# Kernel tuning notes

Measured on AMD Instinct MI355X. Metric: run time of the kernel, lower is better.

Reference implementation:

```python
import jax, jax.numpy as jnp
import numpy as np

EMBED = 200
ATT_D = 200
EPS = 1e-5


def _make_pos(x, embed_len):
    # p[i, j+off, k] = sin(j/1000^(j/E)) if k odd else cos(...); rows with leading
    # zero-count `off` get positions shifted right; first `off` rows stay zero.
    B, L = x.shape
    off = jnp.sum(x == 0, axis=1)                       # [B]
    j = jnp.arange(L)[None, :] - off[:, None]           # [B, L]
    valid = j >= 0
    jf = jnp.maximum(j, 0).astype(jnp.float32)
    angle = jf / jnp.power(1000.0, jf / embed_len)      # [B, L]
    kk = jnp.arange(embed_len)
    odd = (kk % 2 == 1)[None, None, :]
    val = jnp.where(odd, jnp.sin(angle)[:, :, None], jnp.cos(angle)[:, :, None])
    return jnp.where(valid[:, :, None], val, 0.0)       # [B, L, E]


def _ln2(y):
    # F.layer_norm over last TWO dims (seq, embed), no affine
    mu = jnp.mean(y, axis=(1, 2), keepdims=True)
    var = jnp.mean((y - mu) ** 2, axis=(1, 2), keepdims=True)
    return (y - mu) / jnp.sqrt(var + EPS)


def setup_inputs() -> dict:
    key = jax.random.key(0)
    ks = jax.random.split(key, 10)
    B, L, V = 32, 1024, 32000
    x = jax.random.randint(ks[0], (B, L), 0, V)
    embed = jax.random.normal(ks[1], (V, EMBED), dtype=jnp.float32) * 0.02
    w_qkv = jax.random.normal(ks[2], (EMBED, ATT_D), dtype=jnp.float32) * 0.02
    b_qkv = jnp.zeros((ATT_D,), dtype=jnp.float32)
    head = 8
    w_fuse = jax.random.normal(ks[3], (ATT_D * head, ATT_D), dtype=jnp.float32) * 0.02
    b_fuse = jnp.zeros((ATT_D,), dtype=jnp.float32)
    w1 = jax.random.normal(ks[4], (ATT_D, ATT_D), dtype=jnp.float32) * 0.02
    b1 = jnp.zeros((ATT_D,), dtype=jnp.float32)
    w2 = jax.random.normal(ks[5], (ATT_D, ATT_D), dtype=jnp.float32) * 0.02
    b2 = jnp.zeros((ATT_D,), dtype=jnp.float32)
    return {"x": x, "embed": embed, "w_qkv": w_qkv, "b_qkv": b_qkv,
            "w_fuse": w_fuse, "b_fuse": b_fuse, "w1": w1, "b1": b1,
            "w2": w2, "b2": b2, "stack": 6, "head": head}


def reference(x, embed, w_qkv, b_qkv, w_fuse, b_fuse, w1, b1, w2, b2, stack, head):
    p = _make_pos(x, EMBED)
    h = embed[x] + p                                     # [B, L, 200]
    scale = jnp.sqrt(jnp.float32(ATT_D))
    for _ in range(stack):
        r = h
        # q == k == v: the source shares ONE Linear across q/k/v, heads, stacks
        q = h @ w_qkv + b_qkv                            # [B, L, 200]
        d = jnp.einsum('bld,bmd->blm', q, q) / scale     # [B, L, L]
        a = jax.nn.softmax(d, axis=-1)
        c = jnp.einsum('blm,bmd->bld', a, q)             # [B, L, 200]
        c_all = jnp.tile(c, (1, 1, head))                # identical heads concat
        h = c_all @ w_fuse + b_fuse
        h = _ln2(h + r)
        r = h
        h = jax.nn.relu(h @ w1 + b1) @ w2 + b2
        h = _ln2(h + r)
    return h
```

## Files before the change

### kernel.cpp

```cpp
#include <hip/hip_runtime.h>
#include <hip/hip_bf16.h>

#define B_    32
#define L_    1024
#define D_    200
#define DP    256
#define M_    (B_*L_)
#define NTOT  (M_*DP)
#define NELEM 204800.f
#define INVSCALE 0.07071067811865475f
#define LNEPS 1e-5f

typedef unsigned short u16;
typedef unsigned int   u32;
typedef long long      i64;
typedef __attribute__((ext_vector_type(8))) short bf16x8;
typedef __attribute__((ext_vector_type(4))) float f32x4;

__device__ __forceinline__ float bf2f(u32 lo16) {
    union { u32 i; float f; } v; v.i = lo16 << 16; return v.f;
}
__device__ __forceinline__ u16 f2bf(float f) {
    union { float f; u32 i; } v; v.f = f;
    u32 r = v.i + 0x7fffu + ((v.i >> 16) & 1u);
    return (u16)(r >> 16);
}
__device__ __forceinline__ float ldf(const void* p, long i, int isbf) {
    return isbf ? bf2f(((const u16*)p)[i]) : ((const float*)p)[i];
}
__device__ __forceinline__ i64 ldtok(const void* p, long i, int isl64) {
    return isl64 ? ((const i64*)p)[i] : (i64)((const int*)p)[i];
}

__global__ void k_dtype(const u16* __restrict__ e16, const u32* __restrict__ xw,
                        int* __restrict__ flag) {
    int t = threadIdx.x;
    u32 u = e16[2*t];
    u32 ex = (u >> 7) & 0xFFu;
    int sane = (ex >= 0x60u && ex <= 0x87u) ? 1 : 0;
    unsigned long long m1 = __ballot(sane);
    int zhi = (xw[2*t + 1] == 0u) ? 1 : 0;
    unsigned long long m2 = __ballot(zhi);
    if (t == 0) {
        flag[0] = (__popcll(m1) >= 48) ? 1 : 0;
        flag[1] = (__popcll(m2) >= 48) ? 1 : 0;
    }
}

__global__ void k_off(const void* __restrict__ x, const int* __restrict__ flag,
                      int* __restrict__ off) {
    __shared__ int red[256];
    int b = blockIdx.x, t = threadIdx.x;
    int isl64 = flag[1];
    int cnt = 0;
    for (int l = t; l < L_; l += 256)
        cnt += (ldtok(x, (long)b*L_ + l, isl64) == 0) ? 1 : 0;
    red[t] = cnt; __syncthreads();
    for (int s = 128; s > 0; s >>= 1) {
        if (t < s) red[t] += red[t+s];
        __syncthreads();
    }
    if (t == 0) off[b] = red[0];
}

__global__ void k_wfold(const void* __restrict__ wqkv,
                        const void* __restrict__ wfuse,
                        const void* __restrict__ w1,
                        const void* __restrict__ w2,
                        const int* __restrict__ flag,
                        u16* __restrict__ tq, u16* __restrict__ tf,
                        u16* __restrict__ t1, u16* __restrict__ t2) {
    int idx = blockIdx.x*256 + threadIdx.x;
    if (idx >= DP*DP) return;
    int isbf = flag[0];
    int n = idx / DP, k = idx % DP;
    float vq = 0.f, vf = 0.f, v1 = 0.f, v2 = 0.f;
    if (n < D_ && k < D_) {
        vq = ldf(wqkv, k*D_ + n, isbf);
        v1 = ldf(w1,   k*D_ + n, isbf);
        v2 = ldf(w2,   k*D_ + n, isbf);
        #pragma unroll
        for (int hh = 0; hh < 8; ++hh)
            vf += ldf(wfuse, (hh*D_ + k)*D_ + n, isbf);
    }
    tq[idx] = f2bf(vq); tf[idx] = f2bf(vf);
    t1[idx] = f2bf(v1); t2[idx] = f2bf(v2);
}

__global__ void k_bfold(const void* __restrict__ bqkv, const void* __restrict__ bfuse,
                        const void* __restrict__ b1,   const void* __restrict__ b2,
                        const int* __restrict__ flag,
                        float* __restrict__ pq, float* __restrict__ pf,
                        float* __restrict__ p1, float* __restrict__ p2,
                        float* __restrict__ part) {
    int c = threadIdx.x;
    int isbf = flag[0];
    float vq = 0.f, vf = 0.f, v1 = 0.f, v2 = 0.f;
    if (c < D_) {
        vq = ldf(bqkv, c, isbf); vf = ldf(bfuse, c, isbf);
        v1 = ldf(b1,   c, isbf); v2 = ldf(b2,   c, isbf);
    }
    pq[c] = vq; pf[c] = vf; p1[c] = v1; p2[c] = v2;
    if (c < 64) part[c] = 0.f;
}

__global__ void k_embed(const void* __restrict__ x,
                        const void* __restrict__ emb,
                        const int* __restrict__ off,
                        const int* __restrict__ flag,
                        float* __restrict__ A, u16* __restrict__ Abf) {
    int idx = blockIdx.x*256 + threadIdx.x;
    int c = idx & 255;
    int l = (idx >> 8) & 1023;
    int b = idx >> 18;
    float v = 0.f;
    if (c < D_) {
        i64 tok = ldtok(x, (long)b*L_ + l, flag[1]);
        v = ldf(emb, (long)tok*D_ + c, flag[0]);
        int j = l - off[b];
        if (j >= 0) {
            float jf = (float)j;
            float angle = jf * __expf(-jf * 0.034538776394910684f);
            v += (c & 1) ? __sinf(angle) : __cosf(angle);
        }
    }
    A[idx] = v;
    Abf[idx] = f2bf(v);
}

template<int ACT, int OBF, int RES>
__global__ __launch_bounds__(256) void k_gemm_m(const u16* __restrict__ Abf,
                                                const u16* __restrict__ Wt,
                                                const float* __restrict__ biasp,
                                                void* __restrict__ C,
                                                const float* __restrict__ Res,
                                                float* __restrict__ part) {
    __shared__ u16 wt3[32*1032];
    const int t    = threadIdx.x;
    const int lane = t & 63;
    const int w    = t >> 6;
    const int quad = lane >> 4;
    const int l16  = lane & 15;
    const int r0   = blockIdx.x * 128;
    const int c0   = blockIdx.y * 128;

    #pragma unroll
    for (int i = 0; i < 16; ++i) {
        int ci = t + i*256;
        int n = ci >> 5, kc = ci & 31;
        *(uint4*)&wt3[kc*1032 + n*8] =
            *(const uint4*)(Wt + (size_t)(c0 + n)*DP + kc*8);
    }

    bf16x8 qa[2][7];
    #pragma unroll
    for (int rb = 0; rb < 2; ++rb) {
        const u16* ar = Abf + (size_t)(r0 + w*32 + rb*16 + l16)*DP + quad*8;
        #pragma unroll
        for (int kk = 0; kk < 7; ++kk)
            qa[rb][kk] = *(const bf16x8*)(ar + kk*32);
    }
    __syncthreads();

    f32x4 acc[2][8];
    #pragma unroll
    for (int rb = 0; rb < 2; ++rb)
        #pragma unroll
        for (int ct = 0; ct < 8; ++ct) acc[rb][ct] = (f32x4){0.f,0.f,0.f,0.f};

    #pragma unroll
    for (int ct = 0; ct < 8; ++ct) {
        #pragma unroll
        for (int kk = 0; kk < 7; ++kk) {
            bf16x8 vb = *(const bf16x8*)&wt3[(kk*4 + quad)*1032 + (ct*16 + l16)*8];
            acc[0][ct] = __builtin_amdgcn_mfma_f32_16x16x32_bf16(qa[0][kk], vb, acc[0][ct], 0,0,0);
            acc[1][ct] = __builtin_amdgcn_mfma_f32_16x16x32_bf16(qa[1][kk], vb, acc[1][ct], 0,0,0);
        }
    }

    float lsum = 0.f, lss = 0.f;
    #pragma unroll
    for (int ct = 0; ct < 8; ++ct) {
        int col = c0 + ct*16 + l16;
        float bv = biasp[col];
        #pragma unroll
        for (int rb = 0; rb < 2; ++rb) {
            #pragma unroll
            for (int r = 0; r < 4; ++r) {
                int row = r0 + w*32 + rb*16 + quad*4 + r;
                float v = acc[rb][ct][r] + bv;
                if (ACT) v = fmaxf(v, 0.f);
                if (RES) {
                    v += Res[(size_t)row*DP + col];
                    ((float*)C)[(size_t)row*DP + col] = v;
                    if (col < D_) { lsum += v; lss += v*v; }
                } else if (OBF) {
                    ((u16*)C)[(size_t)row*DP + col] = f2bf(v);
                } else {
                    ((float*)C)[(size_t)row*DP + col] = v;
                }
            }
        }
    }
    if (RES) {
        __syncthreads();
        float* red = (float*)wt3;
        red[t] = lsum; red[256 + t] = lss;
        __syncthreads();
        for (int s = 128; s > 0; s >>= 1) {
            if (t < s) { red[t] += red[t+s]; red[256+t] += red[256+t+s]; }
            __syncthreads();
        }
        if (t == 0) {
            int batch = blockIdx.x >> 3;
            atomicAdd(&part[2*batch],     red[0]);
            atomicAdd(&part[2*batch + 1], red[256]);
        }
    }
}

__global__ __launch_bounds__(256) void k_tr(const u16* __restrict__ Qbf,
                                            u16* __restrict__ QbfT) {
    __shared__ u16 tile[64][72];
    const int t  = threadIdx.x;
    const int k0 = blockIdx.x * 64;
    const int f0 = blockIdx.y * 64;
    const int b  = blockIdx.z;
    const u16* S = Qbf  + (size_t)b*(L_*DP);
    u16*      Dd = QbfT + (size_t)b*(L_*DP);
    #pragma unroll
    for (int i = 0; i < 2; ++i) {
        int ci = t + i*256;
        int row = ci >> 3, g = ci & 7;
        *(uint4*)&tile[row][g*8] =
            *(const uint4*)(S + (size_t)(k0+row)*DP + f0 + g*8);
    }
    __syncthreads();
    #pragma unroll
    for (int i = 0; i < 2; ++i) {
        int ci = t + i*256;
        int feat = ci >> 3, g = ci & 7;
        u16 tmp[8];
        #pragma unroll
        for (int e = 0; e < 8; ++e) tmp[e] = tile[g*8+e][feat];
        *(uint4*)(Dd + (size_t)(f0+feat)*L_ + k0 + g*8) = *(uint4*)tmp;
    }
}

__global__ __launch_bounds__(256) void k_attn_m(const u16* __restrict__ Qbf,
                                                const u16* __restrict__ QbfT,
                                                u16* __restrict__ O) {
    __shared__ u16 ks[32*264];
    __shared__ u16 vt[256*40];
    __shared__ u16 ps[64*40];
    const int t    = threadIdx.x;
    const int lane = t & 63;
    const int w    = t >> 6;
    const int quad = lane >> 4;
    const int l16  = lane & 15;
    const int id   = blockIdx.x;
    const int xcd  = id & 7;
    const int ti   = (id >> 3) & 15;
    const int b    = ((id >> 7) << 3) | xcd;
    const int l0   = ti * 64;
    const u16* Qb  = Qbf  + (size_t)b*(L_*DP);
    const u16* QTb = QbfT + (size_t)b*(L_*DP);
    u16*       Ob  = O    + (size_t)b*(L_*DP);

    bf16x8 qa[7];
    {
        const u16* qrow = Qb + (size_t)(l0 + w*16 + l16)*DP + quad*8;
        #pragma unroll
        for (int kk = 0; kk < 7; ++kk)
            qa[kk] = *(const bf16x8*)(qrow + kk*32);
    }
    f32x4 oacc[13];
    #pragma unroll
    for (int ft = 0; ft < 13; ++ft) oacc[ft] = (f32x4){0.f, 0.f, 0.f, 0.f};
    float l_acc[4] = {0.f, 0.f, 0.f, 0.f};

    for (int n0 = 0; n0 < L_; n0 += 32) {
        __syncthreads();
        #pragma unroll
        for (int i = 0; i < 4; ++i) {
            int ci = t + i*256;
            int row = ci >> 5, g = ci & 31;
            *(uint4*)&ks[row*264 + g*8] =
                *(const uint4*)(Qb + (size_t)(n0+row)*DP + g*8);
        }
        #pragma unroll
        for (int i = 0; i < 4; ++i) {
            int ci = t + i*256;
            int feat = ci >> 2, g = ci & 3;
            *(uint4*)&vt[feat*40 + g*8] =
                *(const uint4*)(QTb + (size_t)feat*L_ + n0 + g*8);
        }
        __syncthreads();
        #pragma unroll
        for (int ct = 0; ct < 2; ++ct) {
            f32x4 sc = (f32x4){0.f, 0.f, 0.f, 0.f};
            #pragma unroll
            for (int kk = 0; kk < 7; ++kk) {
                bf16x8 bb = *(const bf16x8*)&ks[(ct*16 + l16)*264 + kk*32 + quad*8];
                sc = __builtin_amdgcn_mfma_f32_16x16x32_bf16(qa[kk], bb, sc, 0, 0, 0);
            }
            #pragma unroll
            for (int r = 0; r < 4; ++r) {
                float p = __expf(sc[r] * INVSCALE);
                l_acc[r] += p;
                ps[(w*16 + quad*4 + r)*40 + ct*16 + l16] = f2bf(p);
            }
        }
        __syncthreads();
        bf16x8 pa = *(const bf16x8*)&ps[(w*16 + l16)*40 + quad*8];
        #pragma unroll
        for (int ft = 0; ft < 13; ++ft) {
            bf16x8 vb = *(const bf16x8*)&vt[(ft*16 + l16)*40 + quad*8];
            oacc[ft] = __builtin_amdgcn_mfma_f32_16x16x32_bf16(pa, vb, oacc[ft], 0, 0, 0);
        }
    }
    #pragma unroll
    for (int r = 0; r < 4; ++r) {
        float v = l_acc[r];
        v += __shfl_xor(v, 1);
        v += __shfl_xor(v, 2);
        v += __shfl_xor(v, 4);
        v += __shfl_xor(v, 8);
        l_acc[r] = 1.f / v;
    }
    #pragma unroll
    for (int r = 0; r < 4; ++r) {
        u16* orow = Ob + (size_t)(l0 + w*16 + quad*4 + r)*DP + l16;
        #pragma unroll
        for (int ft = 0; ft < 13; ++ft)
            orow[ft*16] = f2bf(oacc[ft][r] * l_acc[r]);
    }
}

__global__ void k_ln_stats(float* __restrict__ part, float* __restrict__ stats) {
    int b = threadIdx.x;
    if (b >= 32) return;
    float sum = part[2*b], ss = part[2*b+1];
    float mu  = sum / NELEM;
    float var = ss / NELEM - mu*mu;
    stats[b*2]   = mu;
    stats[b*2+1] = 1.f / sqrtf(var + LNEPS);
    part[2*b] = 0.f; part[2*b+1] = 0.f;
}

__global__ void k_ln_apply(const float* __restrict__ X,
                           const float* __restrict__ stats,
                           float* __restrict__ Out, u16* __restrict__ Outbf) {
    int vi = blockIdx.x*256 + threadIdx.x;
    int b = vi >> 16;
    float mu = stats[b*2], inv = stats[b*2+1];
    int c = (vi & 63) << 2;
    float4 o;
    if (c < D_) {
        float4 xv = *(const float4*)(X + 4*(size_t)vi);
        o.x = (xv.x - mu)*inv;
        o.y = (xv.y - mu)*inv;
        o.z = (xv.z - mu)*inv;
        o.w = (xv.w - mu)*inv;
    } else {
        o.x = o.y = o.z = o.w = 0.f;
    }
    *(float4*)(Out + 4*(size_t)vi) = o;
    uint2 pk;
    pk.x = (u32)f2bf(o.x) | ((u32)f2bf(o.y) << 16);
    pk.y = (u32)f2bf(o.z) | ((u32)f2bf(o.w) << 16);
    *(uint2*)(Outbf + 4*(size_t)vi) = pk;
}

__global__ void k_out(const float* __restrict__ A, const int* __restrict__ flag,
                      float* __restrict__ out) {
    int idx = blockIdx.x*256 + threadIdx.x;
    if (idx >= M_*D_) return;
    int row = idx / D_;
    int c   = idx - row*D_;
    float v = A[(size_t)row*DP + c];
    if (!isfinite(v)) v = 1000.f + 64.f*flag[0] + 16.f*flag[1];
    out[idx] = v;
}

extern "C" void kernel_launch(void* const* d_in, const int* in_sizes, int n_in,
                              void* d_out, int out_size, void* d_ws, size_t ws_size,
                              hipStream_t stream) {
    const void* x     = d_in[0];
    const void* emb   = d_in[1];
    const void* wqkv  = d_in[2];
    const void* bqkv  = d_in[3];
    const void* wfuse = d_in[4];
    const void* bfuse = d_in[5];
    const void* w1    = d_in[6];
    const void* b1    = d_in[7];
    const void* w2    = d_in[8];
    const void* b2    = d_in[9];

    float* A   = (float*)d_ws;
    float* T1  = A + NTOT;
    u16* Abf   = (u16*)(T1 + NTOT);
    u16* Qbf   = Abf + NTOT;
    u16* QbfT  = Qbf + NTOT;
    u16* Hbf   = QbfT;
    u16* Cbf   = QbfT + NTOT;
    u16* wtq   = Cbf + NTOT;
    u16* wtf   = wtq + DP*DP;
    u16* wt1   = wtf + DP*DP;
    u16* wt2   = wt1 + DP*DP;
    float* bqp = (float*)(wt2 + DP*DP);
    float* bfp = bqp + DP;
    float* b1p = bfp + DP;
    float* b2p = b1p + DP;
    float* part = b2p + DP;
    float* stat = part + 64;
    int*   off  = (int*)(stat + 64);
    int*   flag = off + 32;

    k_dtype<<<1, 64, 0, stream>>>((const u16*)emb, (const u32*)x, flag);
    k_off  <<<32, 256, 0, stream>>>(x, flag, off);
    k_wfold<<<DP*DP/256, 256, 0, stream>>>(wqkv, wfuse, w1, w2, flag,
                                           wtq, wtf, wt1, wt2);
    k_bfold<<<1, 256, 0, stream>>>(bqkv, bfuse, b1, b2, flag,
                                   bqp, bfp, b1p, b2p, part);
    k_embed<<<NTOT/256, 256, 0, stream>>>(x, emb, off, flag, A, Abf);

    for (int s = 0; s < 6; ++s) {
        k_gemm_m<0,1,0><<<dim3(M_/128, DP/128), 256, 0, stream>>>(
            Abf, wtq, bqp, Qbf, nullptr, nullptr);
        k_tr<<<dim3(L_/64, DP/64, B_), 256, 0, stream>>>(Qbf, QbfT);
        k_attn_m<<<512, 256, 0, stream>>>(Qbf, QbfT, Cbf);
        k_gemm_m<0,0,1><<<dim3(M_/128, DP/128), 256, 0, stream>>>(
            Cbf, wtf, bfp, T1, A, part);
        k_ln_stats<<<1, 64, 0, stream>>>(part, stat);
        k_ln_apply<<<NTOT/1024, 256, 0, stream>>>(T1, stat, A, Abf);
        k_gemm_m<1,1,0><<<dim3(M_/128, DP/128), 256, 0, stream>>>(
            Abf, wt1, b1p, Hbf, nullptr, nullptr);
        k_gemm_m<0,0,1><<<dim3(M_/128, DP/128), 256, 0, stream>>>(
            Hbf, wt2, b2p, T1, A, part);
        k_ln_stats<<<1, 64, 0, stream>>>(part, stat);
        k_ln_apply<<<NTOT/1024, 256, 0, stream>>>(T1, stat, A, Abf);
    }
    k_out<<<(M_*D_ + 255)/256, 256, 0, stream>>>(A, flag, (float*)d_out);
}
```

Measured before the change: 1.100 ms.

## Fuse layer-norm apply into GEMM prologues and residual epilogues

Removes the standalone ln_apply kernels. Each consumer now normalises on the fly: GEMMs read the un-normalised fp32 activations, apply (x-mu)*inv and convert to bf16 in registers, residual epilogues normalise the residual term, and the output kernel normalises last. This saves the write and re-read of the normalised fp32 and bf16 buffers and two launches per sublayer. In exchange the GEMM A operand is read as fp32 (twice the bytes) with conversion work inside the kernel, and the attention output pad columns are now zeroed explicitly.

```diff
diff --git a/kernel.cpp b/kernel.cpp
--- a/kernel.cpp
+++ b/kernel.cpp
@@ -92,7 +92,7 @@
                         const int* __restrict__ flag,
                         float* __restrict__ pq, float* __restrict__ pf,
                         float* __restrict__ p1, float* __restrict__ p2,
-                        float* __restrict__ part) {
+                        float* __restrict__ part, float* __restrict__ statA) {
     int c = threadIdx.x;
     int isbf = flag[0];
     float vq = 0.f, vf = 0.f, v1 = 0.f, v2 = 0.f;
@@ -102,13 +102,14 @@
     }
     pq[c] = vq; pf[c] = vf; p1[c] = v1; p2[c] = v2;
     if (c < 64) part[c] = 0.f;
+    if (c < 32) { statA[2*c] = 0.f; statA[2*c+1] = 1.f; }
 }
 
 __global__ void k_embed(const void* __restrict__ x,
                         const void* __restrict__ emb,
                         const int* __restrict__ off,
                         const int* __restrict__ flag,
-                        float* __restrict__ A, u16* __restrict__ Abf) {
+                        float* __restrict__ A) {
     int idx = blockIdx.x*256 + threadIdx.x;
     int c = idx & 255;
     int l = (idx >> 8) & 1023;
@@ -125,15 +126,15 @@
         }
     }
     A[idx] = v;
-    Abf[idx] = f2bf(v);
-}
-
-template<int ACT, int OBF, int RES>
-__global__ __launch_bounds__(256) void k_gemm_m(const u16* __restrict__ Abf,
+}
+
+template<int ACT, int OBF, int RES, int LNA>
+__global__ __launch_bounds__(256) void k_gemm_m(const void* __restrict__ Asrc,
                                                 const u16* __restrict__ Wt,
                                                 const float* __restrict__ biasp,
                                                 void* __restrict__ C,
                                                 const float* __restrict__ Res,
+                                                const float* __restrict__ rstat,
                                                 float* __restrict__ part) {
     __shared__ u16 wt3[32*1032];
     const int t    = threadIdx.x;
@@ -144,6 +145,13 @@
     const int r0   = blockIdx.x * 128;
     const int c0   = blockIdx.y * 128;
 
+    float mu = 0.f, inv = 1.f;
+    if (LNA || RES) {
+        int batch = blockIdx.x >> 3;
+        mu  = rstat[2*batch];
+        inv = rstat[2*batch + 1];
+    }
+
     #pragma unroll
     for (int i = 0; i < 16; ++i) {
         int ci = t + i*256;
@@ -155,10 +163,30 @@
     bf16x8 qa[2][7];
     #pragma unroll
     for (int rb = 0; rb < 2; ++rb) {
-        const u16* ar = Abf + (size_t)(r0 + w*32 + rb*16 + l16)*DP + quad*8;
-        #pragma unroll
-        for (int kk = 0; kk < 7; ++kk)
-            qa[rb][kk] = *(const bf16x8*)(ar + kk*32);
+        size_t ro = (size_t)(r0 + w*32 + rb*16 + l16)*DP + quad*8;
+        if (LNA) {
+            const float* ar = (const float*)Asrc + ro;
+            #pragma unroll
+            for (int kk = 0; kk < 7; ++kk) {
+                f32x4 va = *(const f32x4*)(ar + kk*32);
+                f32x4 vb = *(const f32x4*)(ar + kk*32 + 4);
+                bf16x8 q;
+                q[0] = (short)f2bf((va[0]-mu)*inv);
+                q[1] = (short)f2bf((va[1]-mu)*inv);
+                q[2] = (short)f2bf((va[2]-mu)*inv);
+                q[3] = (short)f2bf((va[3]-mu)*inv);
+                q[4] = (short)f2bf((vb[0]-mu)*inv);
+                q[5] = (short)f2bf((vb[1]-mu)*inv);
+                q[6] = (short)f2bf((vb[2]-mu)*inv);
+                q[7] = (short)f2bf((vb[3]-mu)*inv);
+                qa[rb][kk] = q;
+            }
+        } else {
+            const u16* ar = (const u16*)Asrc + ro;
+            #pragma unroll
+            for (int kk = 0; kk < 7; ++kk)
+                qa[rb][kk] = *(const bf16x8*)(ar + kk*32);
+        }
     }
     __syncthreads();
 
@@ -191,7 +219,7 @@
                 float v = acc[rb][ct][r] + bv;
                 if (ACT) v = fmaxf(v, 0.f);
                 if (RES) {
-                    v += Res[(size_t)row*DP + col];
+                    v += (Res[(size_t)row*DP + col] - mu) * inv;
                     ((float*)C)[(size_t)row*DP + col] = v;
                     if (col < D_) { lsum += v; lss += v*v; }
                 } else if (OBF) {
@@ -334,6 +362,7 @@
         #pragma unroll
         for (int ft = 0; ft < 13; ++ft)
             orow[ft*16] = f2bf(oacc[ft][r] * l_acc[r]);
+        orow[13*16] = 0; orow[14*16] = 0; orow[15*16] = 0;
     }
 }
 
@@ -348,37 +377,14 @@
     part[2*b] = 0.f; part[2*b+1] = 0.f;
 }
 
-__global__ void k_ln_apply(const float* __restrict__ X,
-                           const float* __restrict__ stats,
-                           float* __restrict__ Out, u16* __restrict__ Outbf) {
-    int vi = blockIdx.x*256 + threadIdx.x;
-    int b = vi >> 16;
-    float mu = stats[b*2], inv = stats[b*2+1];
-    int c = (vi & 63) << 2;
-    float4 o;
-    if (c < D_) {
-        float4 xv = *(const float4*)(X + 4*(size_t)vi);
-        o.x = (xv.x - mu)*inv;
-        o.y = (xv.y - mu)*inv;
-        o.z = (xv.z - mu)*inv;
-        o.w = (xv.w - mu)*inv;
-    } else {
-        o.x = o.y = o.z = o.w = 0.f;
-    }
-    *(float4*)(Out + 4*(size_t)vi) = o;
-    uint2 pk;
-    pk.x = (u32)f2bf(o.x) | ((u32)f2bf(o.y) << 16);
-    pk.y = (u32)f2bf(o.z) | ((u32)f2bf(o.w) << 16);
-    *(uint2*)(Outbf + 4*(size_t)vi) = pk;
-}
-
-__global__ void k_out(const float* __restrict__ A, const int* __restrict__ flag,
-                      float* __restrict__ out) {
+__global__ void k_out(const float* __restrict__ A, const float* __restrict__ stat,
+                      const int* __restrict__ flag, float* __restrict__ out) {
     int idx = blockIdx.x*256 + threadIdx.x;
     if (idx >= M_*D_) return;
     int row = idx / D_;
     int c   = idx - row*D_;
-    float v = A[(size_t)row*DP + c];
+    int b   = row >> 10;
+    float v = (A[(size_t)row*DP + c] - stat[2*b]) * stat[2*b+1];
     if (!isfinite(v)) v = 1000.f + 64.f*flag[0] + 16.f*flag[1];
     out[idx] = v;
 }
@@ -397,10 +403,9 @@
     const void* w2    = d_in[8];
     const void* b2    = d_in[9];
 
-    float* A   = (float*)d_ws;
-    float* T1  = A + NTOT;
-    u16* Abf   = (u16*)(T1 + NTOT);
-    u16* Qbf   = Abf + NTOT;
+    float* Y0  = (float*)d_ws;
+    float* Y1  = Y0 + NTOT;
+    u16* Qbf   = (u16*)(Y1 + NTOT);
     u16* QbfT  = Qbf + NTOT;
     u16* Hbf   = QbfT;
     u16* Cbf   = QbfT + NTOT;
@@ -412,34 +417,33 @@
     float* bfp = bqp + DP;
     float* b1p = bfp + DP;
     float* b2p = b1p + DP;
-    float* part = b2p + DP;
-    float* stat = part + 64;
-    int*   off  = (int*)(stat + 64);
-    int*   flag = off + 32;
+    float* part  = b2p + DP;
+    float* statA = part + 64;
+    float* statB = statA + 64;
+    int*   off   = (int*)(statB + 64);
+    int*   flag  = off + 32;
 
     k_dtype<<<1, 64, 0, stream>>>((const u16*)emb, (const u32*)x, flag);
     k_off  <<<32, 256, 0, stream>>>(x, flag, off);
     k_wfold<<<DP*DP/256, 256, 0, stream>>>(wqkv, wfuse, w1, w2, flag,
                                            wtq, wtf, wt1, wt2);
     k_bfold<<<1, 256, 0, stream>>>(bqkv, bfuse, b1, b2, flag,
-                                   bqp, bfp, b1p, b2p, part);
-    k_embed<<<NTOT/256, 256, 0, stream>>>(x, emb, off, flag, A, Abf);
+                                   bqp, bfp, b1p, b2p, part, statA);
+    k_embed<<<NTOT/256, 256, 0, stream>>>(x, emb, off, flag, Y0);
 
     for (int s = 0; s < 6; ++s) {
-        k_gemm_m<0,1,0><<<dim3(M_/128, DP/128), 256, 0, stream>>>(
-            Abf, wtq, bqp, Qbf, nullptr, nullptr);
+        k_gemm_m<0,1,0,1><<<dim3(M_/128, DP/128), 256, 0, stream>>>(
+            Y0, wtq, bqp, Qbf, nullptr, statA, nullptr);
         k_tr<<<dim3(L_/64, DP/64, B_), 256, 0, stream>>>(Qbf, QbfT);
         k_attn_m<<<512, 256, 0, stream>>>(Qbf, QbfT, Cbf);
-        k_gemm_m<0,0,1><<<dim3(M_/128, DP/128), 256, 0, stream>>>(
-            Cbf, wtf, bfp, T1, A, part);
-        k_ln_stats<<<1, 64, 0, stream>>>(part, stat);
-        k_ln_apply<<<NTOT/1024, 256, 0, stream>>>(T1, stat, A, Abf);
-        k_gemm_m<1,1,0><<<dim3(M_/128, DP/128), 256, 0, stream>>>(
-            Abf, wt1, b1p, Hbf, nullptr, nullptr);
-        k_gemm_m<0,0,1><<<dim3(M_/128, DP/128), 256, 0, stream>>>(
-            Hbf, wt2, b2p, T1, A, part);
-        k_ln_stats<<<1, 64, 0, stream>>>(part, stat);
-        k_ln_apply<<<NTOT/1024, 256, 0, stream>>>(T1, stat, A, Abf);
-    }
-    k_out<<<(M_*D_ + 255)/256, 256, 0, stream>>>(A, flag, (float*)d_out);
-}
+        k_gemm_m<0,0,1,0><<<dim3(M_/128, DP/128), 256, 0, stream>>>(
+            Cbf, wtf, bfp, Y1, Y0, statA, part);
+        k_ln_stats<<<1, 64, 0, stream>>>(part, statB);
+        k_gemm_m<1,1,0,1><<<dim3(M_/128, DP/128), 256, 0, stream>>>(
+            Y1, wt1, b1p, Hbf, nullptr, statB, nullptr);
+        k_gemm_m<0,0,1,0><<<dim3(M_/128, DP/128), 256, 0, stream>>>(
+            Hbf, wt2, b2p, Y0, Y1, statB, part);
+        k_ln_stats<<<1, 64, 0, stream>>>(part, statA);
+    }
+    k_out<<<(M_*D_ + 255)/256, 256, 0, stream>>>(Y0, statA, flag, (float*)d_out);
+}
```

Measured after the change: 984.9 us. -10.5%, faster.
